# Kernel optimization log

Hardware: AMD Instinct MI355X
Metric: run time of the kernel (lower is better)

## Reference

```python
import jax, jax.numpy as jnp
import numpy as np

BIT_WIDTH = 1
LEVELS = 2 ** BIT_WIDTH - 1
# Floyd-Steinberg gather weights (mirrored scatter kernel): contributions to
# pixel (r,c) from (r-1,c-1), (r-1,c), (r-1,c+1), (r,c-1)
W_UL, W_U, W_UR, W_L = 1.0 / 16, 5.0 / 16, 3.0 / 16, 7.0 / 16


def quant(x):
    return jnp.round(x * LEVELS) / LEVELS


def dither(x01):
    """Raster-scan error-diffusion dithering. x01: [B,C,R,W] in [0,1]."""
    B, C, R, W = x01.shape
    dtype = x01.dtype

    def row_step(prev_err, row_x):
        # prev_err: [B,C,W+2] zero-padded errors of previous row
        # row_x:    [W,B,C]   input values of current row
        up = (W_UL * prev_err[..., 0:W]
              + W_U * prev_err[..., 1:W + 1]
              + W_UR * prev_err[..., 2:W + 2])          # [B,C,W]
        up = jnp.moveaxis(up, -1, 0)                     # [W,B,C]

        def col_step(left_err, xs):
            x, u = xs                                    # each [B,C]
            val = jnp.clip(x + u + W_L * left_err, 0.0, 1.0)
            err = val - quant(val)
            return err, (val, err)

        _, (vals, errs) = jax.lax.scan(col_step, jnp.zeros((B, C), dtype), (row_x, up))
        err_row = jnp.pad(jnp.moveaxis(errs, 0, -1), ((0, 0), (0, 0), (1, 1)))  # [B,C,W+2]
        return err_row, jnp.moveaxis(vals, 0, -1)        # carry, [B,C,W]

    rows_x = jnp.moveaxis(jnp.moveaxis(x01, 2, 0), -1, 1)  # [R,W,B,C]
    init = jnp.zeros((B, C, W + 2), dtype)
    _, out_rows = jax.lax.scan(row_step, init, rows_x)      # [R,B,C,W]
    out = jnp.moveaxis(out_rows, 0, 2)                      # [B,C,R,W]
    return quant(out)


def setup_inputs() -> dict:
    key = jax.random.key(0)
    x = jax.random.normal(key, (32, 3, 512, 512), dtype=jnp.float32)
    return {"x": x}


def reference(x):
    x = jnp.clip(x, -1.0, 1.0)
    x01 = (x + 1.0) / 2.0
    y = dither(x01)
    return y * 2.0 - 1.0
```

## Files before the change

### kernel.cpp

```cpp
#include <hip/hip_runtime.h>


#define F_UL 0.0625f
#define F_U  0.3125f
#define F_UR 0.1875f
#define F_L  0.4375f

typedef unsigned long long ull;

constexpr int WW    = 512;
constexpr int IMG   = WW * WW;
constexpr int NIMG  = 96;
constexpr int NW    = 8;
constexpr int BUFW  = 792;
constexpr int NCH   = 40;
constexpr int LAG   = 10;
constexpr int PPAIR = 320;
constexpr size_t XP_FLOATS = (size_t)NIMG * NW * PPAIR * 128;
constexpr size_t XP_BYTES  = XP_FLOATS * 4;
constexpr size_t XP_SLACK  = 8192;
constexpr size_t XP_OFF    = 4u * 1024 * 1024;
constexpr size_t WS_NEED   = XP_OFF + XP_BYTES + XP_SLACK;

__device__ __forceinline__ float wave_shr1(float v, float fill) {
  int r = __builtin_amdgcn_update_dpp(__float_as_int(fill), __float_as_int(v),
                                      0x138 , 0xF, 0xF, false);
  return __int_as_float(r);
}

__device__ __forceinline__ float pp(float xv) {
#pragma clang fp contract(off)
  float xc = fminf(fmaxf(xv, -1.0f), 1.0f);
  return (xc + 1.0f) * 0.5f;
}

__global__ __launch_bounds__(256)
void pack_kernel(const float* __restrict__ xin, float* __restrict__ xp) {
  __shared__ float ring[4 * 4160];
  const int img = blockIdx.x, w = blockIdx.y;
  const int tid = threadIdx.x;
  const int wv  = tid >> 6, l = tid & 63;

  const float* xg = xin + (size_t)img * IMG + (size_t)w * 64 * WW;
  float* ob = xp + ((size_t)(img * NW + w) * PPAIR) * 128;

  auto load_tile = [&](int t) {
    float* dst = ring + (t & 3) * 4160;
    const float* src = xg + 64 * t;
#pragma unroll
    for (int k = 0; k < 4; ++k) {
      int flat = tid + 256 * k;
      int row = flat >> 4, cq = flat & 15;
      float4 v = *(const float4*)(src + row * WW + cq * 4);
      float* d = dst + row * 65 + cq * 4;
      d[0] = pp(v.x); d[1] = pp(v.y); d[2] = pp(v.z); d[3] = pp(v.w);
    }
  };

  load_tile(0);
  __syncthreads();
  for (int t = 0; t < 10; ++t) {
    if (t < 7) load_tile(t + 1);
    const int Mb = 32 * t + 8 * wv;
#pragma unroll
    for (int i = 0; i < 8; ++i) {
      const int M  = Mb + i;
      const int g  = 2 * (M - l);
      const int gm = g & 511;
      const int idx = ((gm >> 6) & 3) * 4160 + l * 65 + (gm & 63);
      const bool ok = ((unsigned)g < 512u);
      float va = ring[idx], vb = ring[idx + 1];
      float2 v = make_float2(ok ? va : -8.0f, ok ? vb : -8.0f);
      *(float2*)(ob + (size_t)M * 128 + 2 * l) = v;
    }
    __syncthreads();
  }
}

__global__ __launch_bounds__(256, 1)
void dither_packed4(const float* __restrict__ xp, float* __restrict__ yout) {
  __shared__ float bnd[(NW + 1) * BUFW];
  __shared__ int   flags[NW];
  __shared__ ull   bits[NW][11][65];

  const int  tid  = threadIdx.x;
  const int  wave = tid >> 6;
  const int  lane = tid & 63;
  const int  img  = blockIdx.x;
  const bool l63  = (lane == 63);

  for (int i = tid; i < (NW + 1) * BUFW; i += 256) bnd[i] = 0.0f;
  if (tid < NW) flags[tid] = 0;
  bits[wave][10][lane] = 0ull;
  bits[wave + 4][10][lane] = 0ull;
  __syncthreads();

  for (int half = 0; half < 2; ++half) {
    const int p = wave + 4 * half;
    const float* xw = xp + ((size_t)(img * NW + p) * PPAIR) * 128 + lane * 2;
    float* bufR = bnd + p * BUFW;
    float* bufW = bnd + (p + 1) * BUFW;
    ull*   bitp = &bits[p][0][0];

    float2 X0[4], X1[4], X2[4], X3[4], X4[4], X5[4], X6[4], X7[4];
#pragma unroll
    for (int i = 0; i < 4; ++i) {
      X0[i] = *(const float2*)(xw + (size_t)(0  + i) * 128);
      X1[i] = *(const float2*)(xw + (size_t)(4  + i) * 128);
      X2[i] = *(const float2*)(xw + (size_t)(8  + i) * 128);
      X3[i] = *(const float2*)(xw + (size_t)(12 + i) * 128);
    }

    int seen = 0;
    if (p) {
      while ((seen = __hip_atomic_load(&flags[p - 1], __ATOMIC_RELAXED,
                                       __HIP_MEMORY_SCOPE_WORKGROUP)) < LAG)
        __builtin_amdgcn_s_sleep(1);
      __asm__ volatile("s_waitcnt lgkmcnt(0)" ::: "memory");
    }

    float err = 0.0f, s2 = 0.0f;
    float s1 = (lane == 0) ? bufR[129] : 0.0f;
    float2 Q0[4], Q1[4];
#pragma unroll
    for (int i = 0; i < 4; ++i) {
      Q0[i] = *(const float2*)(bufR + 130 + 2 * i);
      Q1[i] = *(const float2*)(bufR + 138 + 2 * i);
    }

    unsigned accLo = 0u, accHi = 0u;

    auto step = [&](float qv, float xv) -> float {
#pragma clang fp contract(off)
      float e_in = wave_shr1(err, qv);
      float t1   = F_UL * s2;
      float t2   = F_U  * s1;
      float t3   = F_UR * e_in;
      float u    = (t1 + t2) + t3;
      float a1   = xv + u;
      float b    = F_L * err;
      float v    = a1 + b;
      float val  = __builtin_amdgcn_fmed3f(v, 0.0f, 1.0f);
      float qn   = rintf(val);
      err = val - qn;
      s2 = s1; s1 = e_in;
      return qn;
    };

    auto iter8 = [&](float2 (&XC)[4], float2 (&XL)[4], float2 (&QC)[4],
                     int T, int bsh, unsigned& acc) {
      const float* lp = xw + (size_t)(T / 2 + 16) * 128;
      XL[0] = *(const float2*)(lp + 0 * 128);
      XL[1] = *(const float2*)(lp + 1 * 128);
      XL[2] = *(const float2*)(lp + 2 * 128);
      XL[3] = *(const float2*)(lp + 3 * 128);

      float p0 = step(QC[0].x, XC[0].x); float e0 = err;
      float p1 = step(QC[0].y, XC[0].y); float e1 = err;
      float p2 = step(QC[1].x, XC[1].x); float e2 = err;
      float p3 = step(QC[1].y, XC[1].y); float e3 = err;
      float p4 = step(QC[2].x, XC[2].x); float e4 = err;
      float p5 = step(QC[2].y, XC[2].y); float e5 = err;
      float p6 = step(QC[3].x, XC[3].x); float e6 = err;
      float p7 = step(QC[3].y, XC[3].y); float e7 = err;

      QC[0] = *(const float2*)(bufR + (T + 146));
      QC[1] = *(const float2*)(bufR + (T + 148));
      QC[2] = *(const float2*)(bufR + (T + 150));
      QC[3] = *(const float2*)(bufR + (T + 152));

      acc |= ((__float_as_uint(p0) >> 29) & 1u) << (bsh + 0);
      acc |= ((__float_as_uint(p1) >> 29) & 1u) << (bsh + 1);
      acc |= ((__float_as_uint(p2) >> 29) & 1u) << (bsh + 2);
      acc |= ((__float_as_uint(p3) >> 29) & 1u) << (bsh + 3);
      acc |= ((__float_as_uint(p4) >> 29) & 1u) << (bsh + 4);
      acc |= ((__float_as_uint(p5) >> 29) & 1u) << (bsh + 5);
      acc |= ((__float_as_uint(p6) >> 29) & 1u) << (bsh + 6);
      acc |= ((__float_as_uint(p7) >> 29) & 1u) << (bsh + 7);

      if (l63) {
        float* bw = bufW + (T + 3);
        bw[0] = e0; bw[1] = e1; bw[2] = e2; bw[3] = e3;
        bw[4] = e4; bw[5] = e5; bw[6] = e6; bw[7] = e7;
      }
    };

    auto waitflag = [&](int j) {
      if (p) {
        int need = j + LAG; if (need > NCH) need = NCH;
        if (seen < need) {
          while ((seen = __hip_atomic_load(&flags[p - 1], __ATOMIC_RELAXED,
                                           __HIP_MEMORY_SCOPE_WORKGROUP)) < need)
            __builtin_amdgcn_s_sleep(1);
          __asm__ volatile("s_waitcnt lgkmcnt(0)" ::: "memory");
        }
      }
    };
    auto pubflag = [&](int v) {
      if (l63) {
        __asm__ volatile("s_waitcnt lgkmcnt(0)" ::: "memory");
        __hip_atomic_store(&flags[p], v, __ATOMIC_RELAXED,
                           __HIP_MEMORY_SCOPE_WORKGROUP);
      }
    };

    for (int jj = 0; jj < NCH; jj += 4) {
      const int T0 = 16 * jj;
      waitflag(jj);
      iter8(X0, X4, Q0, T0 + 0,  0,  accLo);
      iter8(X1, X5, Q1, T0 + 8,  8,  accLo);
      pubflag(jj + 1);
      waitflag(jj + 1);
      iter8(X2, X6, Q0, T0 + 16, 16, accLo);
      iter8(X3, X7, Q1, T0 + 24, 24, accLo);
      pubflag(jj + 2);
      waitflag(jj + 2);
      iter8(X4, X0, Q0, T0 + 32, 0,  accHi);
      iter8(X5, X1, Q1, T0 + 40, 8,  accHi);
      pubflag(jj + 3);
      waitflag(jj + 3);
      iter8(X6, X2, Q0, T0 + 48, 16, accHi);
      iter8(X7, X3, Q1, T0 + 56, 24, accHi);
      pubflag(jj + 4);
      *(uint2*)(bitp + (size_t)(jj >> 2) * 65 + lane) = make_uint2(accLo, accHi);
      accLo = 0u; accHi = 0u;
    }
  }

  for (int half = 0; half < 2; ++half) {
    const int p = wave + 4 * half;
    float* ybase = yout + (size_t)img * IMG + (size_t)(p * 64) * WW + 8 * lane;
    for (int rr = 0; rr < 64; ++rr) {
      const int t0 = 8 * lane + 2 * rr;
      const int t64 = t0 >> 6, sh = t0 & 63;
      ull w1 = bits[p][t64][rr];
      ull w2 = bits[p][t64 + 1][rr];
      unsigned b = (unsigned)((w1 >> sh) | ((w2 << 1) << (63 - sh)));
      float* orow = ybase + (size_t)rr * WW;
      float4 v0, v1;
      v0.x = (b & 1u)   ? 1.0f : -1.0f;
      v0.y = (b & 2u)   ? 1.0f : -1.0f;
      v0.z = (b & 4u)   ? 1.0f : -1.0f;
      v0.w = (b & 8u)   ? 1.0f : -1.0f;
      v1.x = (b & 16u)  ? 1.0f : -1.0f;
      v1.y = (b & 32u)  ? 1.0f : -1.0f;
      v1.z = (b & 64u)  ? 1.0f : -1.0f;
      v1.w = (b & 128u) ? 1.0f : -1.0f;
      *(float4*)(orow)     = v0;
      *(float4*)(orow + 4) = v1;
    }
  }
}

__global__ __launch_bounds__(512, 1)
void dither_direct(const float* __restrict__ xin, float* __restrict__ yout) {
  __shared__ float bnd[(NW + 1) * BUFW];
  __shared__ int flags[NW];

  const int  tid  = threadIdx.x;
  const int  wave = tid >> 6;
  const int  lane = tid & 63;
  const int  img  = blockIdx.x;
  const bool l63  = (lane == 63);

  for (int i = tid; i < (NW + 1) * BUFW; i += 512) bnd[i] = 0.0f;
  if (tid < NW) flags[tid] = 0;
  __syncthreads();

  const int r = wave * 64 + lane;
  const float* xrow = xin + (size_t)img * IMG + (size_t)r * WW;
  float*       yrow = yout + (size_t)img * IMG + (size_t)r * WW;
  float* bufR = bnd + wave * BUFW;
  float* bufW = bnd + (wave + 1) * BUFW;
  const int c0 = -2 * lane;

  auto ldx = [&](int c) -> float2 { return *(const float2*)(xrow + (c & 511)); };

  float2 A0 = ldx(c0 + 0),  A1 = ldx(c0 + 2),  A2 = ldx(c0 + 4),  A3 = ldx(c0 + 6);
  float2 pB0 = ldx(c0 + 8),  pB1 = ldx(c0 + 10), pB2 = ldx(c0 + 12), pB3 = ldx(c0 + 14);
  float2 pC0 = ldx(c0 + 16), pC1 = ldx(c0 + 18), pC2 = ldx(c0 + 20), pC3 = ldx(c0 + 22);
  float xq0 = pp(A0.x), xq1 = pp(A0.y), xq2 = pp(A1.x), xq3 = pp(A1.y);
  float xq4 = pp(A2.x), xq5 = pp(A2.y), xq6 = pp(A3.x), xq7 = pp(A3.y);
  float2 pA0 = pB0, pA1 = pB1, pA2 = pB2, pA3 = pB3;
  pB0 = pC0; pB1 = pC1; pB2 = pC2; pB3 = pC3;

  if (wave) {
    while (__hip_atomic_load(&flags[wave - 1], __ATOMIC_RELAXED,
                             __HIP_MEMORY_SCOPE_WORKGROUP) < LAG)
      __builtin_amdgcn_s_sleep(1);
    __asm__ volatile("s_waitcnt lgkmcnt(0)" ::: "memory");
  }

  float err = 0.0f, s2 = 0.0f;
  float s1 = (lane == 0) ? bufR[129] : 0.0f;
  float2 qa = *(const float2*)(bufR + 130);
  float2 qb = *(const float2*)(bufR + 132);
  float2 qc = *(const float2*)(bufR + 134);
  float2 qd = *(const float2*)(bufR + 136);
  float2 fa = *(const float2*)(bufR + 138);
  float2 fb = *(const float2*)(bufR + 140);
  float2 fc = *(const float2*)(bufR + 142);
  float2 fd = *(const float2*)(bufR + 144);

  auto step = [&](int c, float qv, float xv) -> float {
#pragma clang fp contract(off)
    float e_in = wave_shr1(err, qv);
    float t1   = F_UL * s2;
    float t2   = F_U  * s1;
    float t3   = F_UR * e_in;
    float u    = (t1 + t2) + t3;
    float a1   = xv + u;
    float b    = F_L * err;
    float v    = a1 + b;
    float val  = fminf(fmaxf(v, 0.0f), 1.0f);
    float qn   = rintf(val);
    float e    = val - qn;
    float en   = ((unsigned)c < 512u) ? e : 0.0f;
    err = en; s2 = s1; s1 = e_in;
    return __builtin_fmaf(qn, 2.0f, -1.0f);
  };

  auto iter8 = [&](int T) {
    const int cg = c0 + T;
    float2 n0 = ldx(cg + 24), n1 = ldx(cg + 26), n2 = ldx(cg + 28), n3 = ldx(cg + 30);
    float2 h0 = *(const float2*)(bufR + (T + 146));
    float2 h1 = *(const float2*)(bufR + (T + 148));
    float2 h2 = *(const float2*)(bufR + (T + 150));
    float2 h3 = *(const float2*)(bufR + (T + 152));
    float w0 = pp(pA0.x), w1 = pp(pA0.y), w2 = pp(pA1.x), w3 = pp(pA1.y);
    float w4 = pp(pA2.x), w5 = pp(pA2.y), w6 = pp(pA3.x), w7 = pp(pA3.y);

    float y0 = step(cg + 0, qa.x, xq0); float e0 = err;
    float y1 = step(cg + 1, qa.y, xq1); float e1 = err;
    float y2 = step(cg + 2, qb.x, xq2); float e2 = err;
    float y3 = step(cg + 3, qb.y, xq3); float e3 = err;
    float y4 = step(cg + 4, qc.x, xq4); float e4 = err;
    float y5 = step(cg + 5, qc.y, xq5); float e5 = err;
    float y6 = step(cg + 6, qd.x, xq6); float e6 = err;
    float y7 = step(cg + 7, qd.y, xq7); float e7 = err;

    if ((unsigned)(cg + 0) < 511u) *(float2*)(yrow + cg + 0) = make_float2(y0, y1);
    if ((unsigned)(cg + 2) < 511u) *(float2*)(yrow + cg + 2) = make_float2(y2, y3);
    if ((unsigned)(cg + 4) < 511u) *(float2*)(yrow + cg + 4) = make_float2(y4, y5);
    if ((unsigned)(cg + 6) < 511u) *(float2*)(yrow + cg + 6) = make_float2(y6, y7);

    if (l63) {
      float* bw = bufW + (cg + 129);
      bw[0] = e0; bw[1] = e1; bw[2] = e2; bw[3] = e3;
      bw[4] = e4; bw[5] = e5; bw[6] = e6; bw[7] = e7;
    }

    xq0 = w0; xq1 = w1; xq2 = w2; xq3 = w3;
    xq4 = w4; xq5 = w5; xq6 = w6; xq7 = w7;
    pA0 = pB0; pA1 = pB1; pA2 = pB2; pA3 = pB3;
    pB0 = n0;  pB1 = n1;  pB2 = n2;  pB3 = n3;
    qa = fa; qb = fb; qc = fc; qd = fd;
    fa = h0; fb = h1; fc = h2; fd = h3;
  };

  for (int j = 0; j < NCH; ++j) {
    if (wave) {
      int need = j + LAG; if (need > NCH) need = NCH;
      while (__hip_atomic_load(&flags[wave - 1], __ATOMIC_RELAXED,
                               __HIP_MEMORY_SCOPE_WORKGROUP) < need)
        __builtin_amdgcn_s_sleep(1);
      __asm__ volatile("s_waitcnt lgkmcnt(0)" ::: "memory");
    }
    iter8(16 * j);
    iter8(16 * j + 8);
    if (l63) {
      __asm__ volatile("s_waitcnt lgkmcnt(0)" ::: "memory");
      __hip_atomic_store(&flags[wave], j + 1, __ATOMIC_RELAXED,
                         __HIP_MEMORY_SCOPE_WORKGROUP);
    }
  }
}

extern "C" void kernel_launch(void* const* d_in, const int* in_sizes, int n_in,
                              void* d_out, int out_size, void* d_ws, size_t ws_size,
                              hipStream_t stream) {
  const float* x = (const float*)d_in[0];
  float*       y = (float*)d_out;
  if (ws_size >= WS_NEED) {
    float* xp = (float*)((char*)d_ws + XP_OFF);
    pack_kernel<<<dim3(NIMG, NW), dim3(256), 0, stream>>>(x, xp);
    dither_packed4<<<dim3(NIMG), dim3(256), 0, stream>>>(xp, y);
  } else {
    dither_direct<<<dim3(NIMG), dim3(512), 0, stream>>>(x, y);
  }
}
```

Baseline: 282.7 us.

## Run all eight wavefront stripes concurrently and overlap pack loads with LDS writes

The dither kernel now launches 512 threads so each of the eight 64-row stripes gets its own wave, instead of four waves each processing two stripes one after the other. This removes the serialized second half of the wavefront pipeline, at the cost of more register pressure per SIMD. Bit packing switches from integer shift/or sequences to float multiply-accumulate with power-of-two weights, which are then converted and merged into 64-bit words. The pack kernel splits tile loading into an issue step and a later LDS write step, so the global loads for the next tile can overlap the stores of the current tile.

```diff
diff --git a/kernel.cpp b/kernel.cpp
--- a/kernel.cpp
+++ b/kernel.cpp
@@ -44,23 +44,33 @@
   const float* xg = xin + (size_t)img * IMG + (size_t)w * 64 * WW;
   float* ob = xp + ((size_t)(img * NW + w) * PPAIR) * 128;
 
-  auto load_tile = [&](int t) {
-    float* dst = ring + (t & 3) * 4160;
+  float4 rv[4];
+  auto issue_tile = [&](int t) {
     const float* src = xg + 64 * t;
 #pragma unroll
     for (int k = 0; k < 4; ++k) {
       int flat = tid + 256 * k;
       int row = flat >> 4, cq = flat & 15;
-      float4 v = *(const float4*)(src + row * WW + cq * 4);
+      rv[k] = *(const float4*)(src + row * WW + cq * 4);
+    }
+  };
+  auto write_tile = [&](int t) {
+    float* dst = ring + (t & 3) * 4160;
+#pragma unroll
+    for (int k = 0; k < 4; ++k) {
+      int flat = tid + 256 * k;
+      int row = flat >> 4, cq = flat & 15;
       float* d = dst + row * 65 + cq * 4;
-      d[0] = pp(v.x); d[1] = pp(v.y); d[2] = pp(v.z); d[3] = pp(v.w);
-    }
-  };
-
-  load_tile(0);
+      d[0] = pp(rv[k].x); d[1] = pp(rv[k].y);
+      d[2] = pp(rv[k].z); d[3] = pp(rv[k].w);
+    }
+  };
+
+  issue_tile(0);
+  write_tile(0);
   __syncthreads();
   for (int t = 0; t < 10; ++t) {
-    if (t < 7) load_tile(t + 1);
+    if (t < 7) issue_tile(t + 1);
     const int Mb = 32 * t + 8 * wv;
 #pragma unroll
     for (int i = 0; i < 8; ++i) {
@@ -73,12 +83,13 @@
       float2 v = make_float2(ok ? va : -8.0f, ok ? vb : -8.0f);
       *(float2*)(ob + (size_t)M * 128 + 2 * l) = v;
     }
+    if (t < 7) write_tile(t + 1);
     __syncthreads();
   }
 }
 
-__global__ __launch_bounds__(256, 1)
-void dither_packed4(const float* __restrict__ xp, float* __restrict__ yout) {
+__global__ __launch_bounds__(512, 1)
+void dither_packed(const float* __restrict__ xp, float* __restrict__ yout) {
   __shared__ float bnd[(NW + 1) * BUFW];
   __shared__ int   flags[NW];
   __shared__ ull   bits[NW][11][65];
@@ -89,166 +100,166 @@
   const int  img  = blockIdx.x;
   const bool l63  = (lane == 63);
 
-  for (int i = tid; i < (NW + 1) * BUFW; i += 256) bnd[i] = 0.0f;
+  for (int i = tid; i < (NW + 1) * BUFW; i += 512) bnd[i] = 0.0f;
   if (tid < NW) flags[tid] = 0;
   bits[wave][10][lane] = 0ull;
-  bits[wave + 4][10][lane] = 0ull;
   __syncthreads();
 
-  for (int half = 0; half < 2; ++half) {
-    const int p = wave + 4 * half;
-    const float* xw = xp + ((size_t)(img * NW + p) * PPAIR) * 128 + lane * 2;
-    float* bufR = bnd + p * BUFW;
-    float* bufW = bnd + (p + 1) * BUFW;
-    ull*   bitp = &bits[p][0][0];
-
-    float2 X0[4], X1[4], X2[4], X3[4], X4[4], X5[4], X6[4], X7[4];
+  const float* xw = xp + ((size_t)(img * NW + wave) * PPAIR) * 128 + lane * 2;
+  float* bufR = bnd + wave * BUFW;
+  float* bufW = bnd + (wave + 1) * BUFW;
+
+  float2 X0[4], X1[4], X2[4], X3[4], X4[4], X5[4], X6[4], X7[4];
 #pragma unroll
-    for (int i = 0; i < 4; ++i) {
-      X0[i] = *(const float2*)(xw + (size_t)(0  + i) * 128);
-      X1[i] = *(const float2*)(xw + (size_t)(4  + i) * 128);
-      X2[i] = *(const float2*)(xw + (size_t)(8  + i) * 128);
-      X3[i] = *(const float2*)(xw + (size_t)(12 + i) * 128);
-    }
-
-    int seen = 0;
-    if (p) {
-      while ((seen = __hip_atomic_load(&flags[p - 1], __ATOMIC_RELAXED,
-                                       __HIP_MEMORY_SCOPE_WORKGROUP)) < LAG)
-        __builtin_amdgcn_s_sleep(1);
+  for (int i = 0; i < 4; ++i) {
+    X0[i] = *(const float2*)(xw + (size_t)(0  + i) * 128);
+    X1[i] = *(const float2*)(xw + (size_t)(4  + i) * 128);
+    X2[i] = *(const float2*)(xw + (size_t)(8  + i) * 128);
+    X3[i] = *(const float2*)(xw + (size_t)(12 + i) * 128);
+  }
+
+  int seen = 0;
+  if (wave) {
+    while ((seen = __hip_atomic_load(&flags[wave - 1], __ATOMIC_RELAXED,
+                                     __HIP_MEMORY_SCOPE_WORKGROUP)) < LAG)
+      __builtin_amdgcn_s_sleep(1);
+    __asm__ volatile("s_waitcnt lgkmcnt(0)" ::: "memory");
+  }
+
+  float err = 0.0f, s2 = 0.0f;
+  float s1 = (lane == 0) ? bufR[129] : 0.0f;
+  float2 Q0[4], Q1[4];
+#pragma unroll
+  for (int i = 0; i < 4; ++i) {
+    Q0[i] = *(const float2*)(bufR + 130 + 2 * i);
+    Q1[i] = *(const float2*)(bufR + 138 + 2 * i);
+  }
+
+  float accA = 0.0f, accB = 0.0f, accC = 0.0f;
+
+  auto step = [&](float qv, float xv) -> float {
+#pragma clang fp contract(off)
+    float e_in = wave_shr1(err, qv);
+    float t1   = F_UL * s2;
+    float t2   = F_U  * s1;
+    float t3   = F_UR * e_in;
+    float u    = (t1 + t2) + t3;
+    float a1   = xv + u;
+    float b    = F_L * err;
+    float v    = a1 + b;
+    float val  = __builtin_amdgcn_fmed3f(v, 0.0f, 1.0f);
+    float qn   = rintf(val);
+    err = val - qn;
+    s2 = s1; s1 = e_in;
+    return qn;
+  };
+
+  auto iter8 = [&](float2 (&XC)[4], float2 (&XL)[4], float2 (&QC)[4],
+                   int T, float& acc, float W) {
+    const float* lp = xw + (size_t)(T / 2 + 16) * 128;
+    XL[0] = *(const float2*)(lp + 0 * 128);
+    XL[1] = *(const float2*)(lp + 1 * 128);
+    XL[2] = *(const float2*)(lp + 2 * 128);
+    XL[3] = *(const float2*)(lp + 3 * 128);
+
+    float p0 = step(QC[0].x, XC[0].x); float e0 = err;
+    float p1 = step(QC[0].y, XC[0].y); float e1 = err;
+    float p2 = step(QC[1].x, XC[1].x); float e2 = err;
+    float p3 = step(QC[1].y, XC[1].y); float e3 = err;
+    float p4 = step(QC[2].x, XC[2].x); float e4 = err;
+    float p5 = step(QC[2].y, XC[2].y); float e5 = err;
+    float p6 = step(QC[3].x, XC[3].x); float e6 = err;
+    float p7 = step(QC[3].y, XC[3].y); float e7 = err;
+
+    QC[0] = *(const float2*)(bufR + (T + 146));
+    QC[1] = *(const float2*)(bufR + (T + 148));
+    QC[2] = *(const float2*)(bufR + (T + 150));
+    QC[3] = *(const float2*)(bufR + (T + 152));
+
+    {
+#pragma clang fp contract(off)
+      acc += p0 * (W * 1.0f);
+      acc += p1 * (W * 2.0f);
+      acc += p2 * (W * 4.0f);
+      acc += p3 * (W * 8.0f);
+      acc += p4 * (W * 16.0f);
+      acc += p5 * (W * 32.0f);
+      acc += p6 * (W * 64.0f);
+      acc += p7 * (W * 128.0f);
+    }
+
+    if (l63) {
+      float* bw = bufW + (T + 3);
+      bw[0] = e0; bw[1] = e1; bw[2] = e2; bw[3] = e3;
+      bw[4] = e4; bw[5] = e5; bw[6] = e6; bw[7] = e7;
+    }
+  };
+
+  auto waitflag = [&](int j) {
+    if (wave) {
+      int need = j + LAG; if (need > NCH) need = NCH;
+      if (seen < need) {
+        while ((seen = __hip_atomic_load(&flags[wave - 1], __ATOMIC_RELAXED,
+                                         __HIP_MEMORY_SCOPE_WORKGROUP)) < need)
+          __builtin_amdgcn_s_sleep(1);
+        __asm__ volatile("s_waitcnt lgkmcnt(0)" ::: "memory");
+      }
+    }
+  };
+  auto pubflag = [&](int v) {
+    if (l63) {
       __asm__ volatile("s_waitcnt lgkmcnt(0)" ::: "memory");
-    }
-
-    float err = 0.0f, s2 = 0.0f;
-    float s1 = (lane == 0) ? bufR[129] : 0.0f;
-    float2 Q0[4], Q1[4];
-#pragma unroll
-    for (int i = 0; i < 4; ++i) {
-      Q0[i] = *(const float2*)(bufR + 130 + 2 * i);
-      Q1[i] = *(const float2*)(bufR + 138 + 2 * i);
-    }
-
-    unsigned accLo = 0u, accHi = 0u;
-
-    auto step = [&](float qv, float xv) -> float {
-#pragma clang fp contract(off)
-      float e_in = wave_shr1(err, qv);
-      float t1   = F_UL * s2;
-      float t2   = F_U  * s1;
-      float t3   = F_UR * e_in;
-      float u    = (t1 + t2) + t3;
-      float a1   = xv + u;
-      float b    = F_L * err;
-      float v    = a1 + b;
-      float val  = __builtin_amdgcn_fmed3f(v, 0.0f, 1.0f);
-      float qn   = rintf(val);
-      err = val - qn;
-      s2 = s1; s1 = e_in;
-      return qn;
-    };
-
-    auto iter8 = [&](float2 (&XC)[4], float2 (&XL)[4], float2 (&QC)[4],
-                     int T, int bsh, unsigned& acc) {
-      const float* lp = xw + (size_t)(T / 2 + 16) * 128;
-      XL[0] = *(const float2*)(lp + 0 * 128);
-      XL[1] = *(const float2*)(lp + 1 * 128);
-      XL[2] = *(const float2*)(lp + 2 * 128);
-      XL[3] = *(const float2*)(lp + 3 * 128);
-
-      float p0 = step(QC[0].x, XC[0].x); float e0 = err;
-      float p1 = step(QC[0].y, XC[0].y); float e1 = err;
-      float p2 = step(QC[1].x, XC[1].x); float e2 = err;
-      float p3 = step(QC[1].y, XC[1].y); float e3 = err;
-      float p4 = step(QC[2].x, XC[2].x); float e4 = err;
-      float p5 = step(QC[2].y, XC[2].y); float e5 = err;
-      float p6 = step(QC[3].x, XC[3].x); float e6 = err;
-      float p7 = step(QC[3].y, XC[3].y); float e7 = err;
-
-      QC[0] = *(const float2*)(bufR + (T + 146));
-      QC[1] = *(const float2*)(bufR + (T + 148));
-      QC[2] = *(const float2*)(bufR + (T + 150));
-      QC[3] = *(const float2*)(bufR + (T + 152));
-
-      acc |= ((__float_as_uint(p0) >> 29) & 1u) << (bsh + 0);
-      acc |= ((__float_as_uint(p1) >> 29) & 1u) << (bsh + 1);
-      acc |= ((__float_as_uint(p2) >> 29) & 1u) << (bsh + 2);
-      acc |= ((__float_as_uint(p3) >> 29) & 1u) << (bsh + 3);
-      acc |= ((__float_as_uint(p4) >> 29) & 1u) << (bsh + 4);
-      acc |= ((__float_as_uint(p5) >> 29) & 1u) << (bsh + 5);
-      acc |= ((__float_as_uint(p6) >> 29) & 1u) << (bsh + 6);
-      acc |= ((__float_as_uint(p7) >> 29) & 1u) << (bsh + 7);
-
-      if (l63) {
-        float* bw = bufW + (T + 3);
-        bw[0] = e0; bw[1] = e1; bw[2] = e2; bw[3] = e3;
-        bw[4] = e4; bw[5] = e5; bw[6] = e6; bw[7] = e7;
-      }
-    };
-
-    auto waitflag = [&](int j) {
-      if (p) {
-        int need = j + LAG; if (need > NCH) need = NCH;
-        if (seen < need) {
-          while ((seen = __hip_atomic_load(&flags[p - 1], __ATOMIC_RELAXED,
-                                           __HIP_MEMORY_SCOPE_WORKGROUP)) < need)
-            __builtin_amdgcn_s_sleep(1);
-          __asm__ volatile("s_waitcnt lgkmcnt(0)" ::: "memory");
-        }
-      }
-    };
-    auto pubflag = [&](int v) {
-      if (l63) {
-        __asm__ volatile("s_waitcnt lgkmcnt(0)" ::: "memory");
-        __hip_atomic_store(&flags[p], v, __ATOMIC_RELAXED,
-                           __HIP_MEMORY_SCOPE_WORKGROUP);
-      }
-    };
-
-    for (int jj = 0; jj < NCH; jj += 4) {
-      const int T0 = 16 * jj;
-      waitflag(jj);
-      iter8(X0, X4, Q0, T0 + 0,  0,  accLo);
-      iter8(X1, X5, Q1, T0 + 8,  8,  accLo);
-      pubflag(jj + 1);
-      waitflag(jj + 1);
-      iter8(X2, X6, Q0, T0 + 16, 16, accLo);
-      iter8(X3, X7, Q1, T0 + 24, 24, accLo);
-      pubflag(jj + 2);
-      waitflag(jj + 2);
-      iter8(X4, X0, Q0, T0 + 32, 0,  accHi);
-      iter8(X5, X1, Q1, T0 + 40, 8,  accHi);
-      pubflag(jj + 3);
-      waitflag(jj + 3);
-      iter8(X6, X2, Q0, T0 + 48, 16, accHi);
-      iter8(X7, X3, Q1, T0 + 56, 24, accHi);
-      pubflag(jj + 4);
-      *(uint2*)(bitp + (size_t)(jj >> 2) * 65 + lane) = make_uint2(accLo, accHi);
-      accLo = 0u; accHi = 0u;
-    }
-  }
-
-  for (int half = 0; half < 2; ++half) {
-    const int p = wave + 4 * half;
-    float* ybase = yout + (size_t)img * IMG + (size_t)(p * 64) * WW + 8 * lane;
-    for (int rr = 0; rr < 64; ++rr) {
-      const int t0 = 8 * lane + 2 * rr;
-      const int t64 = t0 >> 6, sh = t0 & 63;
-      ull w1 = bits[p][t64][rr];
-      ull w2 = bits[p][t64 + 1][rr];
-      unsigned b = (unsigned)((w1 >> sh) | ((w2 << 1) << (63 - sh)));
-      float* orow = ybase + (size_t)rr * WW;
-      float4 v0, v1;
-      v0.x = (b & 1u)   ? 1.0f : -1.0f;
-      v0.y = (b & 2u)   ? 1.0f : -1.0f;
-      v0.z = (b & 4u)   ? 1.0f : -1.0f;
-      v0.w = (b & 8u)   ? 1.0f : -1.0f;
-      v1.x = (b & 16u)  ? 1.0f : -1.0f;
-      v1.y = (b & 32u)  ? 1.0f : -1.0f;
-      v1.z = (b & 64u)  ? 1.0f : -1.0f;
-      v1.w = (b & 128u) ? 1.0f : -1.0f;
-      *(float4*)(orow)     = v0;
-      *(float4*)(orow + 4) = v1;
-    }
+      __hip_atomic_store(&flags[wave], v, __ATOMIC_RELAXED,
+                         __HIP_MEMORY_SCOPE_WORKGROUP);
+    }
+  };
+
+  for (int jj = 0; jj < NCH; jj += 4) {
+    const int T0 = 16 * jj;
+    waitflag(jj);
+    iter8(X0, X4, Q0, T0 + 0,  accA, 1.0f);
+    iter8(X1, X5, Q1, T0 + 8,  accA, 256.0f);
+    pubflag(jj + 1);
+    waitflag(jj + 1);
+    iter8(X2, X6, Q0, T0 + 16, accA, 65536.0f);
+    iter8(X3, X7, Q1, T0 + 24, accB, 1.0f);
+    pubflag(jj + 2);
+    waitflag(jj + 2);
+    iter8(X4, X0, Q0, T0 + 32, accB, 256.0f);
+    iter8(X5, X1, Q1, T0 + 40, accB, 65536.0f);
+    pubflag(jj + 3);
+    waitflag(jj + 3);
+    iter8(X6, X2, Q0, T0 + 48, accC, 1.0f);
+    iter8(X7, X3, Q1, T0 + 56, accC, 256.0f);
+    pubflag(jj + 4);
+    unsigned u0 = (unsigned)accA;
+    unsigned u1 = (unsigned)accB;
+    unsigned u2 = (unsigned)accC;
+    unsigned lo = u0 | (u1 << 24);
+    unsigned hi = (u1 >> 8) | (u2 << 16);
+    *(uint2*)&bits[wave][jj >> 2][lane] = make_uint2(lo, hi);
+    accA = 0.0f; accB = 0.0f; accC = 0.0f;
+  }
+
+  float* ybase = yout + (size_t)img * IMG + (size_t)(wave * 64) * WW + 8 * lane;
+  for (int rr = 0; rr < 64; ++rr) {
+    const int t0 = 8 * lane + 2 * rr;
+    const int t64 = t0 >> 6, sh = t0 & 63;
+    ull w1 = bits[wave][t64][rr];
+    ull w2 = bits[wave][t64 + 1][rr];
+    unsigned b = (unsigned)((w1 >> sh) | ((w2 << 1) << (63 - sh)));
+    float* orow = ybase + (size_t)rr * WW;
+    float4 v0, v1;
+    v0.x = (b & 1u)   ? 1.0f : -1.0f;
+    v0.y = (b & 2u)   ? 1.0f : -1.0f;
+    v0.z = (b & 4u)   ? 1.0f : -1.0f;
+    v0.w = (b & 8u)   ? 1.0f : -1.0f;
+    v1.x = (b & 16u)  ? 1.0f : -1.0f;
+    v1.y = (b & 32u)  ? 1.0f : -1.0f;
+    v1.z = (b & 64u)  ? 1.0f : -1.0f;
+    v1.w = (b & 128u) ? 1.0f : -1.0f;
+    *(float4*)(orow)     = v0;
+    *(float4*)(orow + 4) = v1;
   }
 }
 
@@ -384,7 +395,7 @@
   if (ws_size >= WS_NEED) {
     float* xp = (float*)((char*)d_ws + XP_OFF);
     pack_kernel<<<dim3(NIMG, NW), dim3(256), 0, stream>>>(x, xp);
-    dither_packed4<<<dim3(NIMG), dim3(256), 0, stream>>>(xp, y);
+    dither_packed<<<dim3(NIMG), dim3(512), 0, stream>>>(xp, y);
   } else {
     dither_direct<<<dim3(NIMG), dim3(512), 0, stream>>>(x, y);
   }
```

Result: no change. 282.8 us (+0.0%).
